# Performance work log

Measured on AMD Instinct MI355X. Metric: run time of the kernel, lower is better.

## Reference

```python
import jax, jax.numpy as jnp
import numpy as np
import math

B, S, E = 2, 2048, 1024
NH, NKV, HD = 16, 4, 64
GATE_CH = 12

def _rope(x, cos, sin):
    h = x.shape[-1] // 2
    x1, x2 = x[..., :h], x[..., h:]
    return jnp.concatenate((x1 * cos + x2 * sin, x1 * -sin + x2 * cos), axis=-1)

def _rms_norm(x):
    eps = jnp.finfo(x.dtype).eps
    return x * jax.lax.rsqrt(jnp.mean(x * x, axis=-1, keepdims=True) + eps)

def setup_inputs() -> dict:
    key = jax.random.key(0)
    ks = jax.random.split(key, 9)
    x = jax.random.normal(ks[0], (B, S, E), dtype=jnp.float32)
    ve = jax.random.normal(ks[1], (B, S, NKV * HD), dtype=jnp.float32)
    t = jnp.arange(S, dtype=jnp.float32)[:, None]
    inv_freq = 1.0 / (10000.0 ** (jnp.arange(0, HD // 2, dtype=jnp.float32) / (HD // 2)))
    ang = t * inv_freq[None, :]
    cos = jnp.cos(ang)[None, :, None, :]  # (1,S,1,HD//2)
    sin = jnp.sin(ang)[None, :, None, :]
    attn_mask = jnp.tril(jnp.ones((S, S), dtype=bool))[None, None]  # causal (1,1,S,S)
    sc = 0.02
    Wq = jax.random.normal(ks[2], (NH * HD, E), dtype=jnp.float32) * sc
    Wk = jax.random.normal(ks[3], (NKV * HD, E), dtype=jnp.float32) * sc
    Wv = jax.random.normal(ks[4], (NKV * HD, E), dtype=jnp.float32) * sc
    Wproj = jax.random.normal(ks[5], (E, E), dtype=jnp.float32) * sc
    Wgate = jax.random.normal(ks[6], (NKV, GATE_CH), dtype=jnp.float32) * sc
    return {"x": x, "ve": ve, "cos": cos, "sin": sin, "attn_mask": attn_mask,
            "Wq": Wq, "Wk": Wk, "Wv": Wv, "Wproj": Wproj, "Wgate": Wgate}

def reference(x, ve, cos, sin, attn_mask, Wq, Wk, Wv, Wproj, Wgate):
    b, s, _ = x.shape
    q = (x @ Wq.T).reshape(b, s, NH, HD)
    k = (x @ Wk.T).reshape(b, s, NKV, HD)
    v = (x @ Wv.T).reshape(b, s, NKV, HD)
    # value-embedding gating
    gate = 3.0 * jax.nn.sigmoid(x[..., :GATE_CH] @ Wgate.T)  # (b,s,NKV)
    v = v + gate[..., None] * ve.reshape(b, s, NKV, HD)
    # RoPE + QK-RMSNorm
    q = _rms_norm(_rope(q, cos, sin)) * 1.2
    k = _rms_norm(_rope(k, cos, sin)) * 1.2
    # GQA: repeat KV heads
    rep = NH // NKV
    k = jnp.repeat(k, rep, axis=2)
    v = jnp.repeat(v, rep, axis=2)
    q = q.transpose(0, 2, 1, 3)  # (b,h,s,d)
    k = k.transpose(0, 2, 1, 3)
    v = v.transpose(0, 2, 1, 3)
    scores = jnp.einsum('bhqd,bhkd->bhqk', q, k) / math.sqrt(HD)
    scores = jnp.where(attn_mask, scores, jnp.finfo(scores.dtype).min)
    attn = jax.nn.softmax(scores, axis=-1)
    y = jnp.einsum('bhqk,bhkd->bhqd', attn, v)
    y = y.transpose(0, 2, 1, 3).reshape(b, s, NH * HD)
    return y @ Wproj.T
```

## Files before the change

kernel.cpp:

```cpp
#include <hip/hip_runtime.h>
#include <hip/hip_bf16.h>
#include <math.h>

typedef short bf16x8 __attribute__((ext_vector_type(8)));
typedef float f32x4 __attribute__((ext_vector_type(4)));

#define LROW 72

__device__ __forceinline__ unsigned short f2bf(float f) {
  union { float f; unsigned int u; } v; v.f = f;
  unsigned int u = v.u;
  unsigned int r = (u + 0x7fffu + ((u >> 16) & 1u)) >> 16;
  return (unsigned short)r;
}
__device__ __forceinline__ float bf2f(unsigned short u) {
  return __uint_as_float((unsigned)u << 16);
}

#if __has_builtin(__builtin_amdgcn_global_load_lds)
#define HAVE_GLD 1
__device__ __forceinline__ void gld16(const void* g, void* l) {
  __builtin_amdgcn_global_load_lds(
      (const __attribute__((address_space(1))) unsigned int*)g,
      (__attribute__((address_space(3))) unsigned int*)l, 16, 0, 0);
}
#else
#define HAVE_GLD 0
#endif

__global__ __launch_bounds__(256) void cvt_all_kernel(const float* __restrict__ x,
                                                      const float* __restrict__ Wq,
                                                      const float* __restrict__ Wk,
                                                      const float* __restrict__ Wv,
                                                      const float* __restrict__ Wproj,
                                                      unsigned short* __restrict__ xb,
                                                      unsigned short* __restrict__ wqkv,
                                                      unsigned short* __restrict__ wpj) {
  int blk = blockIdx.x;
  const float* src;
  unsigned short* dst;
  if (blk < 4096)      { src = x + (size_t)blk * 1024;            dst = xb + (size_t)blk * 1024; }
  else if (blk < 5120) { src = Wq + (size_t)(blk - 4096) * 1024;  dst = wqkv + (size_t)(blk - 4096) * 1024; }
  else if (blk < 5376) { src = Wk + (size_t)(blk - 5120) * 1024;  dst = wqkv + (size_t)(blk - 4096) * 1024; }
  else if (blk < 5632) { src = Wv + (size_t)(blk - 5376) * 1024;  dst = wqkv + (size_t)(blk - 4096) * 1024; }
  else                 { src = Wproj + (size_t)(blk - 5632) * 1024; dst = wpj + (size_t)(blk - 5632) * 1024; }
  int i = threadIdx.x;
  float4 v = ((const float4*)src)[i];
  ushort4 o;
  o.x = f2bf(v.x); o.y = f2bf(v.y); o.z = f2bf(v.z); o.w = f2bf(v.w);
  ((ushort4*)dst)[i] = o;
}

__global__ __launch_bounds__(256) void gemm_qkv_kernel(const unsigned short* __restrict__ A,
                                                       const unsigned short* __restrict__ B,
                                                       const float* __restrict__ ve,
                                                       const float* __restrict__ cosb,
                                                       const float* __restrict__ sinb,
                                                       const float* __restrict__ wgate,
                                                       unsigned short* __restrict__ Q,
                                                       unsigned short* __restrict__ Kd,
                                                       unsigned short* __restrict__ Vt) {
  __shared__ unsigned short As[64 * 64];
  __shared__ unsigned short Bs[128 * 64];
  __shared__ float gLDS[128];
  const int K = 1024;
  int wg = blockIdx.x;
  int swz = (wg & 7) * 96 + (wg >> 3);
  int n0 = (swz % 12) * 128;
  int m0 = (swz / 12) * 64;
  int tid = threadIdx.x;
  int wave = tid >> 6, lane = tid & 63, l15 = lane & 15, quad = lane >> 4;
  int wm = (wave >> 1) * 32, wn = (wave & 1) * 64;
  if (n0 >= 1280 && tid < 128) {
    int rl = tid & 63, khl = tid >> 6;
    int kh = ((n0 >> 6) - 20) + khl;
    float dot = 0.f;
#pragma unroll
    for (int jj = 0; jj < 12; jj++)
      dot += bf2f(A[(size_t)(m0 + rl) * 1024 + jj]) * wgate[kh * 12 + jj];
    gLDS[khl * 64 + rl] = 3.0f / (1.0f + __expf(-dot));
  }
  f32x4 acc[2][4];
#pragma unroll
  for (int i = 0; i < 2; i++)
#pragma unroll
    for (int j = 0; j < 4; j++) acc[i][j] = (f32x4){0.f, 0.f, 0.f, 0.f};
  int srow = lane >> 3;
  int scol = ((lane & 7) ^ srow) * 8;
  for (int k0 = 0; k0 < K; k0 += 64) {
    __syncthreads();
#if HAVE_GLD
#pragma unroll
    for (int j = 0; j < 2; j++) {
      int row = wave * 16 + j * 8;
      gld16(A + (size_t)(m0 + row + srow) * K + k0 + scol, As + row * 64 + lane * 8);
    }
#pragma unroll
    for (int j = 0; j < 4; j++) {
      int row = wave * 32 + j * 8;
      gld16(B + (size_t)(n0 + row + srow) * K + k0 + scol, Bs + row * 64 + lane * 8);
    }
#else
#pragma unroll
    for (int j = 0; j < 2; j++) {
      int row = wave * 16 + j * 8;
      *(float4*)(As + row * 64 + lane * 8) = *(const float4*)(A + (size_t)(m0 + row + srow) * K + k0 + scol);
    }
#pragma unroll
    for (int j = 0; j < 4; j++) {
      int row = wave * 32 + j * 8;
      *(float4*)(Bs + row * 64 + lane * 8) = *(const float4*)(B + (size_t)(n0 + row + srow) * K + k0 + scol);
    }
#endif
    __syncthreads();
#pragma unroll
    for (int s = 0; s < 2; s++) {
      bf16x8 af[2], bf[4];
#pragma unroll
      for (int i = 0; i < 2; i++)
        af[i] = *(const bf16x8*)(As + (wm + i * 16 + l15) * 64 + (((s * 4 + quad) ^ (l15 & 7)) * 8));
#pragma unroll
      for (int j = 0; j < 4; j++)
        bf[j] = *(const bf16x8*)(Bs + (wn + j * 16 + l15) * 64 + (((s * 4 + quad) ^ (l15 & 7)) * 8));
#pragma unroll
      for (int i = 0; i < 2; i++)
#pragma unroll
        for (int j = 0; j < 4; j++)
          acc[i][j] = __builtin_amdgcn_mfma_f32_16x16x32_bf16(af[i], bf[j], acc[i][j], 0, 0, 0);
    }
  }
  int hs = (n0 + wn) >> 6;
  if (hs < 20) {
    bool isq = hs < 16;
    float postscale = isq ? 0.216404256f : 1.2f;
#pragma unroll
    for (int i = 0; i < 2; i++) {
#pragma unroll
      for (int r = 0; r < 4; r++) {
        int row = m0 + wm + i * 16 + quad * 4 + r;
        int s = row & 2047, b = row >> 11;
        float c0 = cosb[s * 32 + l15],      s0 = sinb[s * 32 + l15];
        float c1 = cosb[s * 32 + 16 + l15], s1 = sinb[s * 32 + 16 + l15];
        float v0 = acc[i][0][r], v1 = acc[i][1][r], v2 = acc[i][2][r], v3 = acc[i][3][r];
        float n0v = fmaf(v0, c0,  v2 * s0);
        float n1v = fmaf(v1, c1,  v3 * s1);
        float n2v = fmaf(v2, c0, -v0 * s0);
        float n3v = fmaf(v3, c1, -v1 * s1);
        float ss = (n0v * n0v + n1v * n1v) + (n2v * n2v + n3v * n3v);
        ss += __shfl_xor(ss, 1, 64); ss += __shfl_xor(ss, 2, 64);
        ss += __shfl_xor(ss, 4, 64); ss += __shfl_xor(ss, 8, 64);
        float sc = rsqrtf(ss * (1.0f / 64.0f) + 1.1920929e-07f) * postscale;
        unsigned short* dp = isq ? Q + ((size_t)(b * 16 + hs) * 2048 + s) * 64
                                 : Kd + ((size_t)(b * 4 + hs - 16) * 2048 + s) * 64;
        dp[l15]      = f2bf(n0v * sc);
        dp[16 + l15] = f2bf(n1v * sc);
        dp[32 + l15] = f2bf(n2v * sc);
        dp[48 + l15] = f2bf(n3v * sc);
      }
    }
  } else {
    int kh = hs - 20;
#pragma unroll
    for (int i = 0; i < 2; i++) {
#pragma unroll
      for (int r = 0; r < 4; r++) {
        int rl = wm + i * 16 + quad * 4 + r;
        int row = m0 + rl, s = row & 2047, b = row >> 11;
        float g = gLDS[(wave & 1) * 64 + rl];
        const float* vep = ve + (size_t)row * 256 + kh * 64;
        unsigned short* vp = Vt + ((size_t)(b * 4 + kh) * 64) * 2048 + s;
#pragma unroll
        for (int j = 0; j < 4; j++) {
          float vv = fmaf(g, vep[j * 16 + l15], acc[i][j][r]);
          vp[(size_t)(j * 16 + l15) * 2048] = f2bf(vv);
        }
      }
    }
  }
}

__global__ __launch_bounds__(256) void flash_kernel(const unsigned short* __restrict__ Q,
                                                    const unsigned short* __restrict__ K,
                                                    const unsigned short* __restrict__ Vt,
                                                    unsigned short* __restrict__ Y) {
  __shared__ unsigned short Ks[64 * 64];
  __shared__ unsigned short Vs[64 * 64];
  __shared__ unsigned short Ps[4 * 16 * LROW];
  int wg = blockIdx.x;
  int swz = (wg & 7) * 64 + (wg >> 3);
  int pair = swz & 15;
  int h = (swz >> 4) & 15;
  int b = swz >> 8;
  int hb = b * 16 + h;
  int kh = h >> 2;
  int tid = threadIdx.x, wave = tid >> 6, lane = tid & 63, l15 = lane & 15, quad = lane >> 4;
  int l7 = l15 & 7;
  const unsigned short* Kg = K + (size_t)(b * 4 + kh) * 2048 * 64;
  const unsigned short* Vg = Vt + (size_t)(b * 4 + kh) * 64 * 2048;
  unsigned short* Pw = Ps + wave * 16 * LROW;
  int row0 = tid >> 3, col8 = (tid & 7) * 8;
  int dchunk = (((tid & 7) ^ (row0 & 7)) * 8);

#pragma unroll
  for (int half = 0; half < 2; half++) {
    int qt = (half == 0) ? pair : 31 - pair;
    int NT = qt + 1;
    int q0 = qt * 64;
    const unsigned short* Qp = Q + (((size_t)hb * 2048) + q0 + wave * 16 + l15) * 64;
    bf16x8 qf0 = *(const bf16x8*)(Qp + quad * 8);
    bf16x8 qf1 = *(const bf16x8*)(Qp + 32 + quad * 8);
    f32x4 acc[4];
#pragma unroll
    for (int i = 0; i < 4; i++) acc[i] = (f32x4){0.f, 0.f, 0.f, 0.f};
    float l_lane = 0.f;

    {
      float4 pk0 = *(const float4*)(Kg + (size_t)row0 * 64 + col8);
      float4 pk1 = *(const float4*)(Kg + (size_t)(row0 + 32) * 64 + col8);
      float4 pv0 = *(const float4*)(Vg + (size_t)row0 * 2048 + col8);
      float4 pv1 = *(const float4*)(Vg + (size_t)(row0 + 32) * 2048 + col8);

      for (int kt = 0; kt < NT; kt++) {
        int k0 = kt * 64;
        __syncthreads();
        *(float4*)(Ks + row0 * 64 + dchunk) = pk0;
        *(float4*)(Ks + (row0 + 32) * 64 + dchunk) = pk1;
        *(float4*)(Vs + row0 * 64 + dchunk) = pv0;
        *(float4*)(Vs + (row0 + 32) * 64 + dchunk) = pv1;
        if (kt + 1 < NT) {
          int kn = k0 + 64;
          pk0 = *(const float4*)(Kg + (size_t)(kn + row0) * 64 + col8);
          pk1 = *(const float4*)(Kg + (size_t)(kn + row0 + 32) * 64 + col8);
          pv0 = *(const float4*)(Vg + (size_t)row0 * 2048 + kn + col8);
          pv1 = *(const float4*)(Vg + (size_t)(row0 + 32) * 2048 + kn + col8);
        }
        __syncthreads();

        f32x4 sv[4];
        __builtin_amdgcn_s_setprio(1);
#pragma unroll
        for (int mt = 0; mt < 4; mt++) {
          sv[mt] = (f32x4){0.f, 0.f, 0.f, 0.f};
          bf16x8 k0f = *(const bf16x8*)(Ks + (mt * 16 + l15) * 64 + ((quad ^ l7) * 8));
          sv[mt] = __builtin_amdgcn_mfma_f32_16x16x32_bf16(k0f, qf0, sv[mt], 0, 0, 0);
          bf16x8 k1f = *(const bf16x8*)(Ks + (mt * 16 + l15) * 64 + (((4 + quad) ^ l7) * 8));
          sv[mt] = __builtin_amdgcn_mfma_f32_16x16x32_bf16(k1f, qf1, sv[mt], 0, 0, 0);
        }
        __builtin_amdgcn_s_setprio(0);
        if (kt == qt) {
          int qg = q0 + wave * 16 + l15;
#pragma unroll
          for (int mt = 0; mt < 4; mt++) {
            int kg = k0 + mt * 16 + quad * 4;
#pragma unroll
            for (int r = 0; r < 4; r++)
              if (kg + r > qg) sv[mt][r] = -1e30f;
          }
        }
#pragma unroll
        for (int mt = 0; mt < 4; mt++) {
          float p0 = __builtin_amdgcn_exp2f(sv[mt][0]);
          float p1 = __builtin_amdgcn_exp2f(sv[mt][1]);
          float p2 = __builtin_amdgcn_exp2f(sv[mt][2]);
          float p3 = __builtin_amdgcn_exp2f(sv[mt][3]);
          l_lane += (p0 + p1) + (p2 + p3);
          unsigned int lo = __builtin_amdgcn_perm(__float_as_uint(p1), __float_as_uint(p0), 0x07060302u);
          unsigned int hi = __builtin_amdgcn_perm(__float_as_uint(p3), __float_as_uint(p2), 0x07060302u);
          *(uint2*)(Pw + l15 * LROW + mt * 16 + quad * 4) = make_uint2(lo, hi);
        }
        __builtin_amdgcn_s_setprio(1);
#pragma unroll
        for (int step = 0; step < 2; step++) {
          bf16x8 pa = *(const bf16x8*)(Pw + l15 * LROW + step * 32 + quad * 8);
#pragma unroll
          for (int nt = 0; nt < 4; nt++) {
            bf16x8 vb = *(const bf16x8*)(Vs + (nt * 16 + l15) * 64 + (((step * 4 + quad) ^ l7) * 8));
            acc[nt] = __builtin_amdgcn_mfma_f32_16x16x32_bf16(pa, vb, acc[nt], 0, 0, 0);
          }
        }
        __builtin_amdgcn_s_setprio(0);
      }
    }
    l_lane += __shfl_xor(l_lane, 16, 64);
    l_lane += __shfl_xor(l_lane, 32, 64);

#pragma unroll
    for (int r = 0; r < 4; r++) {
      float inv = 1.0f / __shfl(l_lane, quad * 4 + r, 16);
      int qrow = q0 + wave * 16 + quad * 4 + r;
      unsigned short* yp = Y + ((size_t)(b * 2048 + qrow) * 1024) + h * 64;
#pragma unroll
      for (int nt = 0; nt < 4; nt++)
        yp[nt * 16 + l15] = f2bf(acc[nt][r] * inv);
    }
  }
}

__global__ __launch_bounds__(256) void gemm_proj_kernel(const unsigned short* __restrict__ A,
                                                        const unsigned short* __restrict__ B,
                                                        float* __restrict__ C) {
  __shared__ unsigned short As[128 * 64];
  __shared__ unsigned short Bs[64 * 64];
  const int K = 1024, N = 1024;
  int wg = blockIdx.x;
  int swz = (wg & 7) * 64 + (wg >> 3);
  int n0 = (swz & 15) * 64;
  int m0 = (swz >> 4) * 128;
  int tid = threadIdx.x;
  int wave = tid >> 6, lane = tid & 63, l15 = lane & 15, quad = lane >> 4;
  int wm = (wave >> 1) * 64, wn = (wave & 1) * 32;
  f32x4 acc[4][2];
#pragma unroll
  for (int i = 0; i < 4; i++)
#pragma unroll
    for (int j = 0; j < 2; j++) acc[i][j] = (f32x4){0.f, 0.f, 0.f, 0.f};
  int srow = lane >> 3;
  int scol = ((lane & 7) ^ srow) * 8;
  for (int k0 = 0; k0 < K; k0 += 64) {
    __syncthreads();
#if HAVE_GLD
#pragma unroll
    for (int j = 0; j < 4; j++) {
      int row = wave * 32 + j * 8;
      gld16(A + (size_t)(m0 + row + srow) * K + k0 + scol, As + row * 64 + lane * 8);
    }
#pragma unroll
    for (int j = 0; j < 2; j++) {
      int row = wave * 16 + j * 8;
      gld16(B + (size_t)(n0 + row + srow) * K + k0 + scol, Bs + row * 64 + lane * 8);
    }
#else
#pragma unroll
    for (int j = 0; j < 4; j++) {
      int row = wave * 32 + j * 8;
      *(float4*)(As + row * 64 + lane * 8) = *(const float4*)(A + (size_t)(m0 + row + srow) * K + k0 + scol);
    }
#pragma unroll
    for (int j = 0; j < 2; j++) {
      int row = wave * 16 + j * 8;
      *(float4*)(Bs + row * 64 + lane * 8) = *(const float4*)(B + (size_t)(n0 + row + srow) * K + k0 + scol);
    }
#endif
    __syncthreads();
#pragma unroll
    for (int s = 0; s < 2; s++) {
      bf16x8 af[4], bf[2];
#pragma unroll
      for (int i = 0; i < 4; i++)
        af[i] = *(const bf16x8*)(As + (wm + i * 16 + l15) * 64 + (((s * 4 + quad) ^ (l15 & 7)) * 8));
#pragma unroll
      for (int j = 0; j < 2; j++)
        bf[j] = *(const bf16x8*)(Bs + (wn + j * 16 + l15) * 64 + (((s * 4 + quad) ^ (l15 & 7)) * 8));
#pragma unroll
      for (int i = 0; i < 4; i++)
#pragma unroll
        for (int j = 0; j < 2; j++)
          acc[i][j] = __builtin_amdgcn_mfma_f32_16x16x32_bf16(af[i], bf[j], acc[i][j], 0, 0, 0);
    }
  }
#pragma unroll
  for (int i = 0; i < 4; i++)
#pragma unroll
    for (int j = 0; j < 2; j++)
#pragma unroll
      for (int r = 0; r < 4; r++)
        C[(size_t)(m0 + wm + i * 16 + quad * 4 + r) * N + n0 + wn + j * 16 + l15] = acc[i][j][r];
}

extern "C" void kernel_launch(void* const* d_in, const int* in_sizes, int n_in,
                              void* d_out, int out_size, void* d_ws, size_t ws_size,
                              hipStream_t stream) {
  const float* x     = (const float*)d_in[0];
  const float* ve    = (const float*)d_in[1];
  const float* cosb  = (const float*)d_in[2];
  const float* sinb  = (const float*)d_in[3];
  const float* Wq    = (const float*)d_in[5];
  const float* Wk    = (const float*)d_in[6];
  const float* Wv    = (const float*)d_in[7];
  const float* Wproj = (const float*)d_in[8];
  const float* Wgate = (const float*)d_in[9];
  float* out = (float*)d_out;
  char* ws = (char*)d_ws;

  size_t o = 0;
  unsigned short* xb   = (unsigned short*)(ws + o); o += (size_t)4096 * 1024 * 2;
  unsigned short* wqkv = (unsigned short*)(ws + o); o += (size_t)1536 * 1024 * 2;
  unsigned short* wpj  = (unsigned short*)(ws + o); o += (size_t)1024 * 1024 * 2;
  unsigned short* Qb   = (unsigned short*)(ws + o); o += (size_t)2 * 16 * 2048 * 64 * 2;
  unsigned short* Kb   = (unsigned short*)(ws + o); o += (size_t)2 * 4 * 2048 * 64 * 2;
  unsigned short* Vb   = (unsigned short*)(ws + o); o += (size_t)2 * 4 * 2048 * 64 * 2;
  unsigned short* Yb   = (unsigned short*)(ws + o); o += (size_t)4096 * 1024 * 2;

  hipLaunchKernelGGL(cvt_all_kernel, dim3(6656), dim3(256), 0, stream,
                     x, Wq, Wk, Wv, Wproj, xb, wqkv, wpj);
  hipLaunchKernelGGL(gemm_qkv_kernel, dim3(768), dim3(256), 0, stream,
                     xb, wqkv, ve, cosb, sinb, Wgate, Qb, Kb, Vb);
  hipLaunchKernelGGL(flash_kernel, dim3(512), dim3(256), 0, stream,
                     Qb, Kb, Vb, Yb);
  hipLaunchKernelGGL(gemm_proj_kernel, dim3(512), dim3(256), 0, stream, Yb, wpj, out);
}
```

Baseline: 169.8 us.

## Fuse paired causal query tiles into one KV sweep sharing K/V loads

Each workgroup previously handled its two query tiles (pair and 31-pair) one after the other, each streaming its own causal range of K/V tiles. It now runs a single KV loop over the longer range and computes both tiles from the same staged K/V in shared memory. The short tile is guarded by a doA predicate, and the P scratch buffer is doubled to hold one slot per tile. This removes the repeated K/V global loads and barriers for the short tile's range. In exchange it doubles the accumulator and Q-fragment registers, which may lower occupancy, and adds branches inside the loop.

```diff
diff --git a/kernel.cpp b/kernel.cpp
--- a/kernel.cpp
+++ b/kernel.cpp
@@ -185,7 +185,7 @@
                                                     unsigned short* __restrict__ Y) {
   __shared__ unsigned short Ks[64 * 64];
   __shared__ unsigned short Vs[64 * 64];
-  __shared__ unsigned short Ps[4 * 16 * LROW];
+  __shared__ unsigned short Ps[4 * 2 * 16 * LROW];
   int wg = blockIdx.x;
   int swz = (wg & 7) * 64 + (wg >> 3);
   int pair = swz & 15;
@@ -197,101 +197,144 @@
   int l7 = l15 & 7;
   const unsigned short* Kg = K + (size_t)(b * 4 + kh) * 2048 * 64;
   const unsigned short* Vg = Vt + (size_t)(b * 4 + kh) * 64 * 2048;
-  unsigned short* Pw = Ps + wave * 16 * LROW;
+  unsigned short* PwA = Ps + (wave * 2 + 0) * 16 * LROW;
+  unsigned short* PwB = Ps + (wave * 2 + 1) * 16 * LROW;
   int row0 = tid >> 3, col8 = (tid & 7) * 8;
   int dchunk = (((tid & 7) ^ (row0 & 7)) * 8);
 
-#pragma unroll
-  for (int half = 0; half < 2; half++) {
-    int qt = (half == 0) ? pair : 31 - pair;
-    int NT = qt + 1;
-    int q0 = qt * 64;
-    const unsigned short* Qp = Q + (((size_t)hb * 2048) + q0 + wave * 16 + l15) * 64;
-    bf16x8 qf0 = *(const bf16x8*)(Qp + quad * 8);
-    bf16x8 qf1 = *(const bf16x8*)(Qp + 32 + quad * 8);
-    f32x4 acc[4];
-#pragma unroll
-    for (int i = 0; i < 4; i++) acc[i] = (f32x4){0.f, 0.f, 0.f, 0.f};
-    float l_lane = 0.f;
-
-    {
-      float4 pk0 = *(const float4*)(Kg + (size_t)row0 * 64 + col8);
-      float4 pk1 = *(const float4*)(Kg + (size_t)(row0 + 32) * 64 + col8);
-      float4 pv0 = *(const float4*)(Vg + (size_t)row0 * 2048 + col8);
-      float4 pv1 = *(const float4*)(Vg + (size_t)(row0 + 32) * 2048 + col8);
-
-      for (int kt = 0; kt < NT; kt++) {
-        int k0 = kt * 64;
-        __syncthreads();
-        *(float4*)(Ks + row0 * 64 + dchunk) = pk0;
-        *(float4*)(Ks + (row0 + 32) * 64 + dchunk) = pk1;
-        *(float4*)(Vs + row0 * 64 + dchunk) = pv0;
-        *(float4*)(Vs + (row0 + 32) * 64 + dchunk) = pv1;
-        if (kt + 1 < NT) {
-          int kn = k0 + 64;
-          pk0 = *(const float4*)(Kg + (size_t)(kn + row0) * 64 + col8);
-          pk1 = *(const float4*)(Kg + (size_t)(kn + row0 + 32) * 64 + col8);
-          pv0 = *(const float4*)(Vg + (size_t)row0 * 2048 + kn + col8);
-          pv1 = *(const float4*)(Vg + (size_t)(row0 + 32) * 2048 + kn + col8);
-        }
-        __syncthreads();
-
-        f32x4 sv[4];
-        __builtin_amdgcn_s_setprio(1);
-#pragma unroll
-        for (int mt = 0; mt < 4; mt++) {
-          sv[mt] = (f32x4){0.f, 0.f, 0.f, 0.f};
-          bf16x8 k0f = *(const bf16x8*)(Ks + (mt * 16 + l15) * 64 + ((quad ^ l7) * 8));
-          sv[mt] = __builtin_amdgcn_mfma_f32_16x16x32_bf16(k0f, qf0, sv[mt], 0, 0, 0);
-          bf16x8 k1f = *(const bf16x8*)(Ks + (mt * 16 + l15) * 64 + (((4 + quad) ^ l7) * 8));
-          sv[mt] = __builtin_amdgcn_mfma_f32_16x16x32_bf16(k1f, qf1, sv[mt], 0, 0, 0);
-        }
-        __builtin_amdgcn_s_setprio(0);
-        if (kt == qt) {
-          int qg = q0 + wave * 16 + l15;
-#pragma unroll
-          for (int mt = 0; mt < 4; mt++) {
-            int kg = k0 + mt * 16 + quad * 4;
-#pragma unroll
-            for (int r = 0; r < 4; r++)
-              if (kg + r > qg) sv[mt][r] = -1e30f;
-          }
-        }
-#pragma unroll
-        for (int mt = 0; mt < 4; mt++) {
-          float p0 = __builtin_amdgcn_exp2f(sv[mt][0]);
-          float p1 = __builtin_amdgcn_exp2f(sv[mt][1]);
-          float p2 = __builtin_amdgcn_exp2f(sv[mt][2]);
-          float p3 = __builtin_amdgcn_exp2f(sv[mt][3]);
-          l_lane += (p0 + p1) + (p2 + p3);
-          unsigned int lo = __builtin_amdgcn_perm(__float_as_uint(p1), __float_as_uint(p0), 0x07060302u);
-          unsigned int hi = __builtin_amdgcn_perm(__float_as_uint(p3), __float_as_uint(p2), 0x07060302u);
-          *(uint2*)(Pw + l15 * LROW + mt * 16 + quad * 4) = make_uint2(lo, hi);
-        }
-        __builtin_amdgcn_s_setprio(1);
-#pragma unroll
-        for (int step = 0; step < 2; step++) {
-          bf16x8 pa = *(const bf16x8*)(Pw + l15 * LROW + step * 32 + quad * 8);
-#pragma unroll
-          for (int nt = 0; nt < 4; nt++) {
-            bf16x8 vb = *(const bf16x8*)(Vs + (nt * 16 + l15) * 64 + (((step * 4 + quad) ^ l7) * 8));
-            acc[nt] = __builtin_amdgcn_mfma_f32_16x16x32_bf16(pa, vb, acc[nt], 0, 0, 0);
-          }
-        }
-        __builtin_amdgcn_s_setprio(0);
-      }
-    }
-    l_lane += __shfl_xor(l_lane, 16, 64);
-    l_lane += __shfl_xor(l_lane, 32, 64);
-
-#pragma unroll
-    for (int r = 0; r < 4; r++) {
-      float inv = 1.0f / __shfl(l_lane, quad * 4 + r, 16);
-      int qrow = q0 + wave * 16 + quad * 4 + r;
-      unsigned short* yp = Y + ((size_t)(b * 2048 + qrow) * 1024) + h * 64;
-#pragma unroll
-      for (int nt = 0; nt < 4; nt++)
-        yp[nt * 16 + l15] = f2bf(acc[nt][r] * inv);
+  int qtA = pair, qtB = 31 - pair;
+  int NTA = qtA + 1, NTB = qtB + 1;
+  int q0A = qtA * 64, q0B = qtB * 64;
+
+  const unsigned short* QpA = Q + (((size_t)hb * 2048) + q0A + wave * 16 + l15) * 64;
+  const unsigned short* QpB = Q + (((size_t)hb * 2048) + q0B + wave * 16 + l15) * 64;
+  bf16x8 qfA0 = *(const bf16x8*)(QpA + quad * 8);
+  bf16x8 qfA1 = *(const bf16x8*)(QpA + 32 + quad * 8);
+  bf16x8 qfB0 = *(const bf16x8*)(QpB + quad * 8);
+  bf16x8 qfB1 = *(const bf16x8*)(QpB + 32 + quad * 8);
+  f32x4 accA[4], accB[4];
+#pragma unroll
+  for (int i = 0; i < 4; i++) {
+    accA[i] = (f32x4){0.f, 0.f, 0.f, 0.f};
+    accB[i] = (f32x4){0.f, 0.f, 0.f, 0.f};
+  }
+  float llA = 0.f, llB = 0.f;
+
+  float4 pk0 = *(const float4*)(Kg + (size_t)row0 * 64 + col8);
+  float4 pk1 = *(const float4*)(Kg + (size_t)(row0 + 32) * 64 + col8);
+  float4 pv0 = *(const float4*)(Vg + (size_t)row0 * 2048 + col8);
+  float4 pv1 = *(const float4*)(Vg + (size_t)(row0 + 32) * 2048 + col8);
+
+  for (int kt = 0; kt < NTB; kt++) {
+    int k0 = kt * 64;
+    __syncthreads();
+    *(float4*)(Ks + row0 * 64 + dchunk) = pk0;
+    *(float4*)(Ks + (row0 + 32) * 64 + dchunk) = pk1;
+    *(float4*)(Vs + row0 * 64 + dchunk) = pv0;
+    *(float4*)(Vs + (row0 + 32) * 64 + dchunk) = pv1;
+    if (kt + 1 < NTB) {
+      int kn = k0 + 64;
+      pk0 = *(const float4*)(Kg + (size_t)(kn + row0) * 64 + col8);
+      pk1 = *(const float4*)(Kg + (size_t)(kn + row0 + 32) * 64 + col8);
+      pv0 = *(const float4*)(Vg + (size_t)row0 * 2048 + kn + col8);
+      pv1 = *(const float4*)(Vg + (size_t)(row0 + 32) * 2048 + kn + col8);
+    }
+    __syncthreads();
+
+    bool doA = (kt < NTA);
+
+    f32x4 svA[4], svB[4];
+    __builtin_amdgcn_s_setprio(1);
+#pragma unroll
+    for (int mt = 0; mt < 4; mt++) {
+      bf16x8 k0f = *(const bf16x8*)(Ks + (mt * 16 + l15) * 64 + ((quad ^ l7) * 8));
+      bf16x8 k1f = *(const bf16x8*)(Ks + (mt * 16 + l15) * 64 + (((4 + quad) ^ l7) * 8));
+      svB[mt] = (f32x4){0.f, 0.f, 0.f, 0.f};
+      svB[mt] = __builtin_amdgcn_mfma_f32_16x16x32_bf16(k0f, qfB0, svB[mt], 0, 0, 0);
+      svB[mt] = __builtin_amdgcn_mfma_f32_16x16x32_bf16(k1f, qfB1, svB[mt], 0, 0, 0);
+      if (doA) {
+        svA[mt] = (f32x4){0.f, 0.f, 0.f, 0.f};
+        svA[mt] = __builtin_amdgcn_mfma_f32_16x16x32_bf16(k0f, qfA0, svA[mt], 0, 0, 0);
+        svA[mt] = __builtin_amdgcn_mfma_f32_16x16x32_bf16(k1f, qfA1, svA[mt], 0, 0, 0);
+      }
+    }
+    __builtin_amdgcn_s_setprio(0);
+    if (kt == qtB) {
+      int qg = q0B + wave * 16 + l15;
+#pragma unroll
+      for (int mt = 0; mt < 4; mt++) {
+        int kg = k0 + mt * 16 + quad * 4;
+#pragma unroll
+        for (int r = 0; r < 4; r++)
+          if (kg + r > qg) svB[mt][r] = -1e30f;
+      }
+    }
+    if (doA && kt == qtA) {
+      int qg = q0A + wave * 16 + l15;
+#pragma unroll
+      for (int mt = 0; mt < 4; mt++) {
+        int kg = k0 + mt * 16 + quad * 4;
+#pragma unroll
+        for (int r = 0; r < 4; r++)
+          if (kg + r > qg) svA[mt][r] = -1e30f;
+      }
+    }
+#pragma unroll
+    for (int mt = 0; mt < 4; mt++) {
+      float p0 = __builtin_amdgcn_exp2f(svB[mt][0]);
+      float p1 = __builtin_amdgcn_exp2f(svB[mt][1]);
+      float p2 = __builtin_amdgcn_exp2f(svB[mt][2]);
+      float p3 = __builtin_amdgcn_exp2f(svB[mt][3]);
+      llB += (p0 + p1) + (p2 + p3);
+      unsigned int lo = __builtin_amdgcn_perm(__float_as_uint(p1), __float_as_uint(p0), 0x07060302u);
+      unsigned int hi = __builtin_amdgcn_perm(__float_as_uint(p3), __float_as_uint(p2), 0x07060302u);
+      *(uint2*)(PwB + l15 * LROW + mt * 16 + quad * 4) = make_uint2(lo, hi);
+    }
+    if (doA) {
+#pragma unroll
+      for (int mt = 0; mt < 4; mt++) {
+        float p0 = __builtin_amdgcn_exp2f(svA[mt][0]);
+        float p1 = __builtin_amdgcn_exp2f(svA[mt][1]);
+        float p2 = __builtin_amdgcn_exp2f(svA[mt][2]);
+        float p3 = __builtin_amdgcn_exp2f(svA[mt][3]);
+        llA += (p0 + p1) + (p2 + p3);
+        unsigned int lo = __builtin_amdgcn_perm(__float_as_uint(p1), __float_as_uint(p0), 0x07060302u);
+        unsigned int hi = __builtin_amdgcn_perm(__float_as_uint(p3), __float_as_uint(p2), 0x07060302u);
+        *(uint2*)(PwA + l15 * LROW + mt * 16 + quad * 4) = make_uint2(lo, hi);
+      }
+    }
+    __builtin_amdgcn_s_setprio(1);
+#pragma unroll
+    for (int step = 0; step < 2; step++) {
+      bf16x8 paB = *(const bf16x8*)(PwB + l15 * LROW + step * 32 + quad * 8);
+      bf16x8 paA;
+      if (doA) paA = *(const bf16x8*)(PwA + l15 * LROW + step * 32 + quad * 8);
+#pragma unroll
+      for (int nt = 0; nt < 4; nt++) {
+        bf16x8 vb = *(const bf16x8*)(Vs + (nt * 16 + l15) * 64 + (((step * 4 + quad) ^ l7) * 8));
+        accB[nt] = __builtin_amdgcn_mfma_f32_16x16x32_bf16(paB, vb, accB[nt], 0, 0, 0);
+        if (doA) accA[nt] = __builtin_amdgcn_mfma_f32_16x16x32_bf16(paA, vb, accA[nt], 0, 0, 0);
+      }
+    }
+    __builtin_amdgcn_s_setprio(0);
+  }
+
+  llA += __shfl_xor(llA, 16, 64);
+  llA += __shfl_xor(llA, 32, 64);
+  llB += __shfl_xor(llB, 16, 64);
+  llB += __shfl_xor(llB, 32, 64);
+#pragma unroll
+  for (int r = 0; r < 4; r++) {
+    float invA = 1.0f / __shfl(llA, quad * 4 + r, 16);
+    float invB = 1.0f / __shfl(llB, quad * 4 + r, 16);
+    int qrA = q0A + wave * 16 + quad * 4 + r;
+    int qrB = q0B + wave * 16 + quad * 4 + r;
+    unsigned short* ypA = Y + ((size_t)(b * 2048 + qrA) * 1024) + h * 64;
+    unsigned short* ypB = Y + ((size_t)(b * 2048 + qrB) * 1024) + h * 64;
+#pragma unroll
+    for (int nt = 0; nt < 4; nt++) {
+      ypA[nt * 16 + l15] = f2bf(accA[nt][r] * invA);
+      ypB[nt * 16 + l15] = f2bf(accB[nt][r] * invB);
     }
   }
 }
```

Measured after the change: 180.2 us. +6.1%, slower.
